# Performance work log

Hardware: AMD Instinct MI355X
Metric: run time of the kernel (lower is better)

The kernel has to match this reference:

```python
import jax, jax.numpy as jnp
import numpy as np

EPS = 1e-5
NH = 8          # num_heads
WT_LEVELS = 5


def ln(x, w, b):
    m = jnp.mean(x, -1, keepdims=True)
    v = jnp.mean((x - m) ** 2, -1, keepdims=True)
    return (x - m) / jnp.sqrt(v + EPS) * w + b


def gelu(x):
    return jax.nn.gelu(x, approximate=False)  # torch nn.GELU default (erf)


def dwconv(x, w, b, stride, padding):
    # x: [B,C,H,W], w: [kh,kw,1,C] depthwise
    C = x.shape[1]
    y = jax.lax.conv_general_dilated(x, w, (stride, stride), padding,
                                     dimension_numbers=('NCHW', 'HWIO', 'NCHW'),
                                     feature_group_count=C)
    return y if b is None else y + b[None, :, None, None]


def conv2d(x, w, b, padding='SAME'):
    y = jax.lax.conv_general_dilated(x, w, (1, 1), padding,
                                     dimension_numbers=('NCHW', 'HWIO', 'NCHW'))
    return y + b[None, :, None, None]


def haar_dwt(x):
    # orthonormal 2x2 Haar analysis via even/odd slicing (no conv needed)
    a = x[..., 0::2, 0::2]; b = x[..., 0::2, 1::2]
    c = x[..., 1::2, 0::2]; d = x[..., 1::2, 1::2]
    ll = (a + b + c + d) * 0.5
    lh = (-a - b + c + d) * 0.5
    hl = (-a + b - c + d) * 0.5
    hh = (a - b - c + d) * 0.5
    return ll, lh, hl, hh


def haar_idwt(ll, lh, hl, hh):
    a = (ll - lh - hl + hh) * 0.5
    b = (ll - lh + hl - hh) * 0.5
    c = (ll + lh - hl - hh) * 0.5
    d = (ll + lh + hl + hh) * 0.5
    B, C, H, W = ll.shape
    top = jnp.stack([a, b], -1).reshape(B, C, H, 2 * W)
    bot = jnp.stack([c, d], -1).reshape(B, C, H, 2 * W)
    return jnp.stack([top, bot], -2).reshape(B, C, 2 * H, 2 * W)


def wtconv(x, base_w, base_b, base_scale, wav_w, wav_scale):
    # WTConv2d (Haar, wt_levels=5, kernel 3, depthwise): multi-level wavelet
    # decomposition, depthwise 3x3 conv + scale at each level, reconstruction,
    # added to a scaled depthwise base conv.
    B, C = x.shape[0], x.shape[1]
    lls, hs, shapes = [], [], []
    cur = x
    for i in range(WT_LEVELS):
        shapes.append(cur.shape)
        Hc, Wc = cur.shape[2], cur.shape[3]
        if Hc % 2 or Wc % 2:
            cur = jnp.pad(cur, ((0, 0), (0, 0), (0, Hc % 2), (0, Wc % 2)))
        sub = jnp.stack(haar_dwt(cur), 2)                # [B,C,4,h,w]
        cur = sub[:, :, 0]
        h, w = sub.shape[3], sub.shape[4]
        t = sub.reshape(B, C * 4, h, w)
        t = dwconv(t, wav_w[i], None, 1, 'SAME') * wav_scale[i][None, :, None, None]
        t = t.reshape(B, C, 4, h, w)
        lls.append(t[:, :, 0])
        hs.append(t[:, :, 1:4])
    nxt = 0.0
    for i in range(WT_LEVELS - 1, -1, -1):
        ll = lls[i] + nxt
        h3 = hs[i]
        nxt = haar_idwt(ll, h3[:, :, 0], h3[:, :, 1], h3[:, :, 2])
        sh = shapes[i]
        nxt = nxt[:, :, :sh[2], :sh[3]]
    base = dwconv(x, base_w, base_b, 1, 'SAME') * base_scale[None, :, None, None]
    return base + nxt


def block_forward(x, H, W, ln1_w, ln1_b, ln2_w, ln2_b, q_w, kv1_w, kv2_w,
                  sr1_w, sr1_b, sr2_w, sr2_b, an1_w, an1_b, an2_w, an2_b,
                  wt_base_w, wt_base_b, wt_base_scale, wt_wav_w, wt_wav_scale,
                  cp2d_w, cp2d_b, cn_w, cn_b, proj_w, proj_b,
                  fc1_w, fc1_b, fc2_w, fc2_b):
    B, N, C0 = x.shape
    Cp = C0 // 4            # conv/wavelet part channels
    Ca = C0 - Cp            # attention part channels (3/4)
    hd = Ca // NH
    scale = hd ** -0.5

    xin = ln(x, ln1_w, ln1_b)
    xc, xa = xin[..., :Cp], xin[..., Cp:]

    # --- wavelet-conv branch ---
    xc = xc.reshape(B, H, W, Cp).transpose(0, 3, 1, 2)        # [B,Cp,H,W]
    xc = wtconv(xc, wt_base_w, wt_base_b, wt_base_scale, wt_wav_w, wt_wav_scale)
    xc = conv2d(xc, cp2d_w, cp2d_b, 'SAME')                   # k3 p1 (sr_ratio=8)
    xc = gelu(ln(xc.reshape(B, Cp, N).transpose(0, 2, 1), cn_w, cn_b))  # [B,N,Cp]

    # --- multi-scale spatial-reduction attention (sr_ratio=8) ---
    q = (xa @ q_w).reshape(B, N, NH, hd).transpose(0, 2, 1, 3)  # [B,NH,N,hd]
    x_ = xa.transpose(0, 2, 1).reshape(B, Ca, H, W)
    x1 = gelu(ln(dwconv(x_, sr1_w, sr1_b, 8, 'VALID').reshape(B, Ca, -1)
                 .transpose(0, 2, 1), an1_w, an1_b))           # [B,49,Ca]
    x2 = gelu(ln(dwconv(x_, sr2_w, sr2_b, 4, 'VALID').reshape(B, Ca, -1)
                 .transpose(0, 2, 1), an2_w, an2_b))           # [B,196,Ca]

    def branch(xs, kv_w, qh):
        L = xs.shape[1]
        kv = (xs @ kv_w).reshape(B, L, 2, NH // 2, hd).transpose(2, 0, 3, 1, 4)
        k, v = kv[0], kv[1]
        a = jax.nn.softmax(jnp.einsum('bhnd,bhld->bhnl', qh, k) * scale, axis=-1)
        return jnp.einsum('bhnl,bhld->bhnd', a, v).transpose(0, 2, 1, 3).reshape(B, N, Ca // 2)

    y1 = branch(x1, kv1_w, q[:, :NH // 2])
    y2 = branch(x2, kv2_w, q[:, NH // 2:])

    attn_out = jnp.concatenate([y1, y2, xc], -1) @ proj_w + proj_b

    x = x + attn_out
    m = ln(x, ln2_w, ln2_b)
    return x + (gelu(m @ fc1_w + fc1_b) @ fc2_w + fc2_b)


def setup_inputs() -> dict:
    key = jax.random.key(0)
    ks = jax.random.split(key, 16)
    B, H, W, C0 = 32, 56, 56, 128
    N = H * W
    Cp, Ca = C0 // 4, C0 // 4 * 3

    def nrm(k, shape, std=0.02):
        return jax.random.normal(k, shape, jnp.float32) * std

    return dict(
        x=jax.random.normal(ks[0], (B, N, C0), jnp.float32),
        H=H, W=W,
        ln1_w=jnp.ones((C0,)), ln1_b=jnp.zeros((C0,)),
        ln2_w=jnp.ones((C0,)), ln2_b=jnp.zeros((C0,)),
        q_w=nrm(ks[1], (Ca, Ca)),
        kv1_w=nrm(ks[2], (Ca, Ca)),
        kv2_w=nrm(ks[3], (Ca, Ca)),
        sr1_w=nrm(ks[4], (8, 8, 1, Ca), 0.05), sr1_b=jnp.zeros((Ca,)),
        sr2_w=nrm(ks[5], (4, 4, 1, Ca), 0.05), sr2_b=jnp.zeros((Ca,)),
        an1_w=jnp.ones((Ca,)), an1_b=jnp.zeros((Ca,)),
        an2_w=jnp.ones((Ca,)), an2_b=jnp.zeros((Ca,)),
        wt_base_w=nrm(ks[6], (3, 3, 1, Cp), 0.1), wt_base_b=jnp.zeros((Cp,)),
        wt_base_scale=jnp.ones((Cp,)),
        wt_wav_w=nrm(ks[7], (5, 3, 3, 1, 4 * Cp), 0.1),
        wt_wav_scale=jnp.full((5, 4 * Cp), 0.1, jnp.float32),
        cp2d_w=nrm(ks[8], (3, 3, Cp, Cp), 0.05), cp2d_b=jnp.zeros((Cp,)),
        cn_w=jnp.ones((Cp,)), cn_b=jnp.zeros((Cp,)),
        proj_w=nrm(ks[9], (C0, C0)), proj_b=jnp.zeros((C0,)),
        fc1_w=nrm(ks[10], (C0, 4 * C0)), fc1_b=jnp.zeros((4 * C0,)),
        fc2_w=nrm(ks[11], (4 * C0, C0)), fc2_b=jnp.zeros((C0,)),
    )


def reference(x, H, W, ln1_w, ln1_b, ln2_w, ln2_b, q_w, kv1_w, kv2_w,
              sr1_w, sr1_b, sr2_w, sr2_b, an1_w, an1_b, an2_w, an2_b,
              wt_base_w, wt_base_b, wt_base_scale, wt_wav_w, wt_wav_scale,
              cp2d_w, cp2d_b, cn_w, cn_b, proj_w, proj_b,
              fc1_w, fc1_b, fc2_w, fc2_b):
    return block_forward(x, H, W, ln1_w, ln1_b, ln2_w, ln2_b, q_w, kv1_w, kv2_w,
                         sr1_w, sr1_b, sr2_w, sr2_b, an1_w, an1_b, an2_w, an2_b,
                         wt_base_w, wt_base_b, wt_base_scale, wt_wav_w, wt_wav_scale,
                         cp2d_w, cp2d_b, cn_w, cn_b, proj_w, proj_b,
                         fc1_w, fc1_b, fc2_w, fc2_b)
```

## Files before the change

kernel.cpp:

```cpp
#include <hip/hip_runtime.h>
#include <hip/hip_bf16.h>
#include <math.h>

typedef __hip_bfloat16 bf16;
typedef __attribute__((ext_vector_type(8))) short bf16x8;
typedef __attribute__((ext_vector_type(4))) float f32x4;

#define Bc   32
#define Hc   56
#define Wcc  56
#define Nc   3136
#define Cpc  32
#define Cac  96
#define EPSc 1e-5f
#define SCALEc 0.28867513459481287f

__device__ __forceinline__ float gelu_f(float x) {
    return 0.5f * x * (1.0f + erff(x * 0.7071067811865475f));
}

__device__ __forceinline__ float fast_exp2(float x) {
#if defined(__has_builtin)
#if __has_builtin(__builtin_amdgcn_exp2f)
    return __builtin_amdgcn_exp2f(x);
#else
    return exp2f(x);
#endif
#else
    return exp2f(x);
#endif
}

__global__ __launch_bounds__(256) void ln1_kernel(const float* __restrict__ x,
        const float* __restrict__ g, const float* __restrict__ be,
        float* __restrict__ xa, bf16* __restrict__ xab, float* __restrict__ xc_img)
{
    int wv = threadIdx.x >> 6, lane = threadIdx.x & 63;
    int row = blockIdx.x * 4 + wv;
    if (row >= Bc * Nc) return;
    const float* xr = x + (size_t)row * 128;
    float x0 = xr[lane];
    float x1 = xr[lane + 64];
    float s = x0 + x1, q = x0 * x0 + x1 * x1;
    for (int o = 32; o; o >>= 1) { s += __shfl_xor(s, o); q += __shfl_xor(q, o); }
    float mean = s * (1.f / 128.f);
    float inv = rsqrtf(q * (1.f / 128.f) - mean * mean + EPSc);
    int b = row / Nc, n = row % Nc;
    {
        int c = lane;
        float y = (x0 - mean) * inv * g[c] + be[c];
        if (c < Cpc) xc_img[(size_t)(b * Cpc + c) * Nc + n] = y;
        else { xa[(size_t)row * Cac + (c - Cpc)] = y;
               xab[(size_t)row * Cac + (c - Cpc)] = __float2bfloat16(y); }
    }
    {
        int c = lane + 64;
        float y = (x1 - mean) * inv * g[c] + be[c];
        xa[(size_t)row * Cac + (c - Cpc)] = y;
        xab[(size_t)row * Cac + (c - Cpc)] = __float2bfloat16(y);
    }
}

__global__ void dwt_kernel(const float* __restrict__ src, int cs, int h, int w,
                           int h2, int w2, float* __restrict__ sub)
{
    int t = blockIdx.x * blockDim.x + threadIdx.x;
    int total = Bc * 32 * h2 * w2;
    if (t >= total) return;
    int xx = t % w2; int r = t / w2;
    int yy = r % h2; r /= h2;
    int c = r & 31; int b = r >> 5;
    const float* sp = src + (size_t)cs * (b * 32 + c) * h * w;
    int y0 = yy * 2, x0 = xx * 2;
    bool xe = (x0 + 1 < w), ye = (y0 + 1 < h);
    float a  = sp[y0 * w + x0];
    float bb = xe ? sp[y0 * w + x0 + 1] : 0.f;
    float cc = ye ? sp[(y0 + 1) * w + x0] : 0.f;
    float dd = (xe && ye) ? sp[(y0 + 1) * w + x0 + 1] : 0.f;
    size_t pl = (size_t)h2 * w2;
    size_t ob = (size_t)(b * 128 + c * 4) * pl + yy * w2 + xx;
    sub[ob]          = ( a + bb + cc + dd) * 0.5f;
    sub[ob + pl]     = (-a - bb + cc + dd) * 0.5f;
    sub[ob + 2 * pl] = (-a + bb - cc + dd) * 0.5f;
    sub[ob + 3 * pl] = ( a - bb - cc + dd) * 0.5f;
}

template<int H>
__device__ __forceinline__ void dw3_body(int r, const float* __restrict__ src,
        const float* __restrict__ wt, const float* __restrict__ scale,
        float* __restrict__ dst)
{
    int x = r % H; int rr = r / H;
    int y = rr % H; rr /= H;
    int c = rr & 127;
    const float* sp = src + (r - x - y * H);
    float acc = 0.f;
    #pragma unroll
    for (int u = 0; u < 3; u++) {
        int yy = y + u - 1;
        if (yy < 0 || yy >= H) continue;
        #pragma unroll
        for (int v = 0; v < 3; v++) {
            int xx = x + v - 1;
            if (xx < 0 || xx >= H) continue;
            acc += sp[yy * H + xx] * wt[(u * 3 + v) * 128 + c];
        }
    }
    dst[r] = acc * scale[c];
}

__global__ void dw3x3_all_kernel(const float* __restrict__ sub, const float* __restrict__ wavw,
        const float* __restrict__ wavs, float* __restrict__ tt)
{
    int t = blockIdx.x * blockDim.x + threadIdx.x;
    if (t < 3211264)      dw3_body<28>(t,           sub,           wavw,        wavs,       tt);
    else if (t < 4014080) dw3_body<14>(t - 3211264, sub + 3211264, wavw + 1152, wavs + 128, tt + 3211264);
    else if (t < 4214784) dw3_body<7> (t - 4014080, sub + 4014080, wavw + 2304, wavs + 256, tt + 4014080);
    else if (t < 4280320) dw3_body<4> (t - 4214784, sub + 4214784, wavw + 3456, wavs + 384, tt + 4214784);
    else if (t < 4296704) dw3_body<2> (t - 4280320, sub + 4280320, wavw + 4608, wavs + 512, tt + 4280320);
}

__global__ void idwt_kernel(const float* __restrict__ tl, const float* __restrict__ nxt,
        float* __restrict__ outp, int h2, int w2, int ho, int wo)
{
    int t = blockIdx.x * blockDim.x + threadIdx.x;
    int total = Bc * 32 * ho * wo;
    if (t >= total) return;
    int x = t % wo; int r = t / wo;
    int y = r % ho; r /= ho;
    int c = r & 31; int b = r >> 5;
    int y2 = y >> 1, x2 = x >> 1;
    size_t pl = (size_t)h2 * w2;
    size_t base = (size_t)(b * 128 + c * 4) * pl + y2 * w2 + x2;
    float ll = tl[base];
    if (nxt) ll += nxt[(size_t)(b * 32 + c) * pl + y2 * w2 + x2];
    float lh = tl[base + pl], hl = tl[base + 2 * pl], hh = tl[base + 3 * pl];
    float v;
    if ((y & 1) == 0) v = ((x & 1) == 0) ? (ll - lh - hl + hh) : (ll - lh + hl - hh);
    else              v = ((x & 1) == 0) ? (ll + lh - hl - hh) : (ll + lh + hl + hh);
    outp[t] = v * 0.5f;
}

__global__ void idwt_dwbase_kernel(const float* __restrict__ tl, const float* __restrict__ nxt,
        const float* __restrict__ src, const float* __restrict__ wt,
        const float* __restrict__ scale, const float* __restrict__ bias,
        bf16* __restrict__ dst_nhwc)
{
    int t = blockIdx.x * blockDim.x + threadIdx.x;
    if (t >= Bc * 32 * Nc) return;
    int x = t % Wcc; int r = t / Wcc;
    int y = r % Hc; r /= Hc;
    int c = r & 31; int b = r >> 5;
    int y2 = y >> 1, x2 = x >> 1;
    const size_t pl = 784;
    size_t base = (size_t)(b * 128 + c * 4) * pl + y2 * 28 + x2;
    float ll = tl[base] + nxt[(size_t)(b * 32 + c) * pl + y2 * 28 + x2];
    float lh = tl[base + pl], hl = tl[base + 2 * pl], hh = tl[base + 3 * pl];
    float v;
    if ((y & 1) == 0) v = ((x & 1) == 0) ? (ll - lh - hl + hh) : (ll - lh + hl - hh);
    else              v = ((x & 1) == 0) ? (ll + lh - hl - hh) : (ll + lh + hl + hh);
    float recon = v * 0.5f;
    const float* sp = src + (t - x - y * Wcc);
    float acc = 0.f;
    #pragma unroll
    for (int u = 0; u < 3; u++) {
        int yy = y + u - 1;
        if (yy < 0 || yy >= Hc) continue;
        #pragma unroll
        for (int vv2 = 0; vv2 < 3; vv2++) {
            int xx = x + vv2 - 1;
            if (xx < 0 || xx >= Wcc) continue;
            acc += sp[yy * Wcc + xx] * wt[(u * 3 + vv2) * 32 + c];
        }
    }
    acc = (acc + bias[c]) * scale[c] + recon;
    dst_nhwc[(((size_t)b * Hc + y) * Wcc + x) * 32 + c] = __float2bfloat16(acc);
}

__global__ void wprep_kernel(const float* __restrict__ qw, const float* __restrict__ kv1w,
        const float* __restrict__ kv2w, const float* __restrict__ pw,
        const float* __restrict__ f1w, const float* __restrict__ f2w,
        const float* __restrict__ cpw, bf16* __restrict__ qwt, bf16* __restrict__ kv1wt,
        bf16* __restrict__ kv2wt, bf16* __restrict__ pwt, bf16* __restrict__ w1t,
        bf16* __restrict__ w2t, bf16* __restrict__ cpwt)
{
    int t = blockIdx.x * blockDim.x + threadIdx.x;
    if (t < 9216) {
        int n = t % 96, k = t / 96;
        qwt[n * 96 + k] = __float2bfloat16(qw[t]);
    } else if (t < 18432) {
        int u = t - 9216; int n = u % 96, k = u / 96;
        kv1wt[n * 96 + k] = __float2bfloat16(kv1w[u]);
    } else if (t < 27648) {
        int u = t - 18432; int n = u % 96, k = u / 96;
        kv2wt[n * 96 + k] = __float2bfloat16(kv2w[u]);
    } else if (t < 44032) {
        int u = t - 27648; int n = u % 128, k = u / 128;
        pwt[n * 128 + k] = __float2bfloat16(pw[u]);
    } else if (t < 109568) {
        int u = t - 44032; int n = u % 512, k = u / 512;
        w1t[(size_t)n * 128 + k] = __float2bfloat16(f1w[u]);
    } else if (t < 175104) {
        int u = t - 109568; int n = u % 128, k = u / 128;
        w2t[(size_t)n * 512 + k] = __float2bfloat16(f2w[u]);
    } else if (t < 184320) {
        int u = t - 175104; int co = u / 288, k = u % 288;
        cpwt[u] = __float2bfloat16(cpw[k * 32 + co]);
    }
}

__global__ __launch_bounds__(256) void cp2d_cn_kernel(const bf16* __restrict__ src,
        const bf16* __restrict__ wtc, const float* __restrict__ bias,
        const float* __restrict__ cnw, const float* __restrict__ cnb,
        bf16* __restrict__ attn_cat)
{
    __shared__ unsigned short in_s[10 * 400];
    __shared__ unsigned short w_s[32 * 296];
    int tid = threadIdx.x;
    int b = blockIdx.y;
    int ty = blockIdx.x / 7, tx = blockIdx.x % 7;
    for (int idx = tid; idx < 1152; idx += 256) {
        int co = idx / 36, j8 = (idx % 36) * 8;
        *(int4*)&w_s[co * 296 + j8] = *(const int4*)(wtc + co * 288 + j8);
    }
    {
        int idx = tid;
        if (idx < 200) {
            int cell = idx >> 1, half = idx & 1;
            int dy = cell / 10, dx = cell % 10;
            int gy = ty * 8 - 1 + dy, gx = tx * 8 - 1 + dx;
            int4 v0 = make_int4(0, 0, 0, 0), v1 = v0;
            if (gy >= 0 && gy < 56 && gx >= 0 && gx < 56) {
                const int4* gp = (const int4*)(src + ((((size_t)b * 56 + gy) * 56 + gx) * 32 + half * 16));
                v0 = gp[0]; v1 = gp[1];
            }
            *(int4*)&in_s[dy * 400 + dx * 40 + half * 16] = v0;
            *(int4*)&in_s[dy * 400 + dx * 40 + half * 16 + 8] = v1;
        }
    }
    __syncthreads();
    int wave = tid >> 6, lane = tid & 63;
    int ml = lane & 15, qd = lane >> 4;
    int m = wave * 16 + ml;
    int ly = m >> 3, lx = m & 7;
    f32x4 acc0 = {0.f, 0.f, 0.f, 0.f}, acc1 = {0.f, 0.f, 0.f, 0.f};
    #pragma unroll
    for (int u = 0; u < 3; u++)
    #pragma unroll
    for (int v = 0; v < 3; v++) {
        bf16x8 af = *(const bf16x8*)&in_s[(ly + u) * 400 + (lx + v) * 40 + qd * 8];
        int k = (u * 3 + v) * 32 + qd * 8;
        bf16x8 b0 = *(const bf16x8*)&w_s[ml * 296 + k];
        bf16x8 b1 = *(const bf16x8*)&w_s[(16 + ml) * 296 + k];
        acc0 = __builtin_amdgcn_mfma_f32_16x16x32_bf16(af, b0, acc0, 0, 0, 0);
        acc1 = __builtin_amdgcn_mfma_f32_16x16x32_bf16(af, b1, acc1, 0, 0, 0);
    }
    float bia0 = bias[ml], bia1 = bias[16 + ml];
    float g0 = cnw[ml], g1 = cnw[16 + ml];
    float be0 = cnb[ml], be1 = cnb[16 + ml];
    #pragma unroll
    for (int r = 0; r < 4; r++) {
        float c0 = acc0[r] + bia0;
        float c1 = acc1[r] + bia1;
        float s = c0 + c1, q = c0 * c0 + c1 * c1;
        #pragma unroll
        for (int o = 8; o; o >>= 1) { s += __shfl_xor(s, o); q += __shfl_xor(q, o); }
        float mean = s * (1.f / 32.f);
        float inv = rsqrtf(q * (1.f / 32.f) - mean * mean + EPSc);
        int mr = wave * 16 + qd * 4 + r;
        int ry = ty * 8 + (mr >> 3), rx = tx * 8 + (mr & 7);
        bf16* op = attn_cat + ((size_t)b * Nc + ry * 56 + rx) * 128 + 96;
        op[ml]      = __float2bfloat16(gelu_f((c0 - mean) * inv * g0 + be0));
        op[16 + ml] = __float2bfloat16(gelu_f((c1 - mean) * inv * g1 + be1));
    }
}

template<int KS, int LD>
__device__ __forceinline__ void sr_body(int t, const float* __restrict__ xa,
        const float* __restrict__ wt, const float* __restrict__ bias,
        float* __restrict__ outp)
{
    int c = t % Cac; int r = t / Cac;
    int j = r % LD; r /= LD;
    int i = r % LD; int b = r / LD;
    float acc = bias[c];
    for (int u = 0; u < KS; u++)
        for (int v = 0; v < KS; v++)
            acc += xa[(size_t)(b * Nc + (i * KS + u) * Wcc + (j * KS + v)) * Cac + c]
                 * wt[(u * KS + v) * Cac + c];
    outp[t] = acc;
}

__global__ void sr_all_kernel(const float* __restrict__ xa,
        const float* __restrict__ sr1w, const float* __restrict__ sr1b, float* __restrict__ x1p,
        const float* __restrict__ sr2w, const float* __restrict__ sr2b, float* __restrict__ x2p)
{
    int t = blockIdx.x * blockDim.x + threadIdx.x;
    if (t < 150528) sr_body<8, 7>(t, xa, sr1w, sr1b, x1p);
    else {
        int u = t - 150528;
        if (u < 602112) sr_body<4, 14>(u, xa, sr2w, sr2b, x2p);
    }
}

__global__ __launch_bounds__(256) void ln96_all_kernel(
        const float* __restrict__ s1, const float* __restrict__ g1,
        const float* __restrict__ b1, bf16* __restrict__ d1,
        const float* __restrict__ s2, const float* __restrict__ g2,
        const float* __restrict__ b2, bf16* __restrict__ d2)
{
    int wv = threadIdx.x >> 6, lane = threadIdx.x & 63;
    int row = blockIdx.x * 4 + wv;
    const float* sp; const float* g; const float* be; bf16* dst; int r;
    if (row < 1568)      { sp = s1; g = g1; be = b1; dst = d1; r = row; }
    else if (row < 7840) { sp = s2; g = g2; be = b2; dst = d2; r = row - 1568; }
    else return;
    sp += (size_t)r * 96;
    float x0 = sp[lane];
    float x1 = (lane < 32) ? sp[64 + lane] : 0.f;
    float s = x0 + x1, q = x0 * x0 + x1 * x1;
    for (int o = 32; o; o >>= 1) { s += __shfl_xor(s, o); q += __shfl_xor(q, o); }
    float mean = s * (1.f / 96.f);
    float inv = rsqrtf(q * (1.f / 96.f) - mean * mean + EPSc);
    dst[(size_t)r * 96 + lane] =
        __float2bfloat16(gelu_f((x0 - mean) * inv * g[lane] + be[lane]));
    if (lane < 32)
        dst[(size_t)r * 96 + 64 + lane] =
            __float2bfloat16(gelu_f((x1 - mean) * inv * g[64 + lane] + be[64 + lane]));
}

template<int NF, int BK, bool GELU, bool RES, int OMODE>
__global__ __launch_bounds__(256) void gemm_kernel(const bf16* __restrict__ A,
        const bf16* __restrict__ Wt, const float* __restrict__ bias,
        const float* __restrict__ res, void* __restrict__ outp,
        int M, int K, int Nt)
{
    constexpr int TN = 16 * NF;
    __shared__ unsigned short As[64][BK + 8];
    __shared__ unsigned short Bs[TN][BK + 8];
    int tid = threadIdx.x;
    int wave = tid >> 6, lane = tid & 63;
    int m0 = blockIdx.y * 64, n0 = blockIdx.x * TN;
    f32x4 acc[NF];
    #pragma unroll
    for (int f = 0; f < NF; f++) acc[f] = (f32x4){0.f, 0.f, 0.f, 0.f};

    int ar = tid >> 2, ac = (tid & 3) << 3;
    int ml = wave * 16 + (lane & 15);
    int qd = lane >> 4;

    for (int k0 = 0; k0 < K; k0 += BK) {
        #pragma unroll
        for (int i = 0; i < BK / 32; i++) {
            int cc = ac + i * 32;
            int4 av = make_int4(0, 0, 0, 0);
            if (m0 + ar < M) av = *(const int4*)(A + (size_t)(m0 + ar) * K + k0 + cc);
            *(int4*)&As[ar][cc] = av;
        }
        for (int idx = tid; idx < TN * (BK / 8); idx += 256) {
            int br = idx / (BK / 8), bc = (idx % (BK / 8)) * 8;
            *(int4*)&Bs[br][bc] = *(const int4*)(Wt + (size_t)(n0 + br) * K + k0 + bc);
        }
        __syncthreads();
        #pragma unroll
        for (int kk = 0; kk < BK / 32; kk++) {
            bf16x8 af = *(const bf16x8*)&As[ml][kk * 32 + qd * 8];
            #pragma unroll
            for (int f = 0; f < NF; f++) {
                bf16x8 bfv = *(const bf16x8*)&Bs[f * 16 + (lane & 15)][kk * 32 + qd * 8];
                acc[f] = __builtin_amdgcn_mfma_f32_16x16x32_bf16(af, bfv, acc[f], 0, 0, 0);
            }
        }
        __syncthreads();
    }
    #pragma unroll
    for (int f = 0; f < NF; f++) {
        int n = n0 + f * 16 + (lane & 15);
        #pragma unroll
        for (int r = 0; r < 4; r++) {
            int m = m0 + wave * 16 + qd * 4 + r;
            if (m >= M) continue;
            float v = acc[f][r];
            if (bias) v += bias[n];
            if (GELU) v = gelu_f(v);
            if (RES)  v += res[(size_t)m * Nt + n];
            if (OMODE == 1)
                ((bf16*)outp)[(size_t)m * Nt + n] = __float2bfloat16(v);
            else if (OMODE == 2) {
                int b = m / Nc, nn = m - b * Nc;
                int h = n / 12, d = n - h * 12;
                ((float*)outp)[(((size_t)(b * 8 + h)) * Nc + nn) * 12 + d] = v;
            } else
                ((float*)outp)[(size_t)m * Nt + n] = v;
        }
    }
}

__global__ __launch_bounds__(256) void proj_ln_kernel(const bf16* __restrict__ A,
        const bf16* __restrict__ Wt, const float* __restrict__ bias,
        const float* __restrict__ res, const float* __restrict__ g,
        const float* __restrict__ be, float* __restrict__ xres, bf16* __restrict__ xnb)
{
    __shared__ unsigned short As[64][72];
    __shared__ unsigned short Bs[128][72];
    int tid = threadIdx.x;
    int wave = tid >> 6, lane = tid & 63;
    int m0 = blockIdx.x * 64;
    f32x4 acc[8];
    #pragma unroll
    for (int f = 0; f < 8; f++) acc[f] = (f32x4){0.f, 0.f, 0.f, 0.f};

    int ar = tid >> 2, ac = (tid & 3) << 3;
    int ml = lane & 15, qd = lane >> 4;
    int mlw = wave * 16 + ml;

    for (int k0 = 0; k0 < 128; k0 += 64) {
        #pragma unroll
        for (int i = 0; i < 2; i++) {
            int cc = ac + i * 32;
            *(int4*)&As[ar][cc] = *(const int4*)(A + (size_t)(m0 + ar) * 128 + k0 + cc);
        }
        for (int idx = tid; idx < 1024; idx += 256) {
            int br = idx >> 3, bc = (idx & 7) * 8;
            *(int4*)&Bs[br][bc] = *(const int4*)(Wt + (size_t)br * 128 + k0 + bc);
        }
        __syncthreads();
        #pragma unroll
        for (int kk = 0; kk < 2; kk++) {
            bf16x8 af = *(const bf16x8*)&As[mlw][kk * 32 + qd * 8];
            #pragma unroll
            for (int f = 0; f < 8; f++) {
                bf16x8 bfv = *(const bf16x8*)&Bs[f * 16 + ml][kk * 32 + qd * 8];
                acc[f] = __builtin_amdgcn_mfma_f32_16x16x32_bf16(af, bfv, acc[f], 0, 0, 0);
            }
        }
        __syncthreads();
    }
    float bia[8], gg[8], bb[8];
    #pragma unroll
    for (int f = 0; f < 8; f++) {
        int n = f * 16 + ml;
        bia[f] = bias[n]; gg[f] = g[n]; bb[f] = be[n];
    }
    #pragma unroll
    for (int r = 0; r < 4; r++) {
        int m = m0 + wave * 16 + qd * 4 + r;
        float vv[8];
        float s = 0.f, q = 0.f;
        #pragma unroll
        for (int f = 0; f < 8; f++) {
            int n = f * 16 + ml;
            float v = acc[f][r] + bia[f] + res[(size_t)m * 128 + n];
            vv[f] = v; s += v; q += v * v;
        }
        #pragma unroll
        for (int o = 8; o; o >>= 1) { s += __shfl_xor(s, o); q += __shfl_xor(q, o); }
        float mean = s * (1.f / 128.f);
        float inv = rsqrtf(q * (1.f / 128.f) - mean * mean + EPSc);
        #pragma unroll
        for (int f = 0; f < 8; f++) {
            int n = f * 16 + ml;
            xres[(size_t)m * 128 + n] = vv[f];
            xnb[(size_t)m * 128 + n] =
                __float2bfloat16((vv[f] - mean) * inv * gg[f] + bb[f]);
        }
    }
}

template<int L>
__device__ __forceinline__ void attn_body(const float* __restrict__ qh,
        const float* __restrict__ kv, int hl, int h, int b,
        float* kb, float* vb, bf16* __restrict__ attn_cat)
{
    for (int idx = threadIdx.x; idx < L * 3; idx += 256) {
        int l = idx / 3, f = idx % 3;
        const float4* kp = (const float4*)(kv + (size_t)(b * L + l) * 96 + hl * 12) + f;
        float4 kk = kp[0];
        float4 vv = kp[12];
        *(float4*)&kb[l * 12 + f * 4] = kk;
        *(float4*)&vb[l * 12 + f * 4] = vv;
    }
    int n = blockIdx.x * 256 + threadIdx.x;
    bool act = (n < Nc);
    int nn = act ? n : (Nc - 1);
    const float4* qp = (const float4*)(qh + (((size_t)(b * 8 + h)) * Nc + nn) * 12);
    float4 q0 = qp[0], q1 = qp[1], q2 = qp[2];
    const float PRE = SCALEc * 1.4426950408889634f;
    q0.x *= PRE; q0.y *= PRE; q0.z *= PRE; q0.w *= PRE;
    q1.x *= PRE; q1.y *= PRE; q1.z *= PRE; q1.w *= PRE;
    q2.x *= PRE; q2.y *= PRE; q2.z *= PRE; q2.w *= PRE;
    __syncthreads();

    float den = 0.f;
    float o[12];
    #pragma unroll
    for (int d = 0; d < 12; d++) o[d] = 0.f;

    #pragma unroll 4
    for (int l = 0; l < L; l++) {
        const float4 k0 = *(const float4*)&kb[l * 12];
        const float4 k1 = *(const float4*)&kb[l * 12 + 4];
        const float4 k2 = *(const float4*)&kb[l * 12 + 8];
        float s0 = q0.x * k0.x + q0.y * k0.y + q0.z * k0.z + q0.w * k0.w;
        float s1 = q1.x * k1.x + q1.y * k1.y + q1.z * k1.z + q1.w * k1.w;
        float s2 = q2.x * k2.x + q2.y * k2.y + q2.z * k2.z + q2.w * k2.w;
        float e = fast_exp2(s0 + s1 + s2);
        den += e;
        const float4 v0 = *(const float4*)&vb[l * 12];
        const float4 v1 = *(const float4*)&vb[l * 12 + 4];
        const float4 v2 = *(const float4*)&vb[l * 12 + 8];
        o[0] += e * v0.x; o[1]  += e * v0.y; o[2]  += e * v0.z; o[3]  += e * v0.w;
        o[4] += e * v1.x; o[5]  += e * v1.y; o[6]  += e * v1.z; o[7]  += e * v1.w;
        o[8] += e * v2.x; o[9]  += e * v2.y; o[10] += e * v2.z; o[11] += e * v2.w;
    }
    if (act) {
        float rden = 1.f / den;
        bf16* op = attn_cat + (size_t)(b * Nc + n) * 128 + h * 12;
        #pragma unroll
        for (int d = 0; d < 12; d++) op[d] = __float2bfloat16(o[d] * rden);
    }
}

__global__ __launch_bounds__(256) void attn_kernel(const float* __restrict__ qh,
        const float* __restrict__ kv1, const float* __restrict__ kv2,
        bf16* __restrict__ attn_cat)
{
    __shared__ float kb[196 * 12];
    __shared__ float vb[196 * 12];
    int h = blockIdx.y, b = blockIdx.z;
    if (h < 4) attn_body<49> (qh, kv1, h,     h, b, kb, vb, attn_cat);
    else       attn_body<196>(qh, kv2, h - 4, h, b, kb, vb, attn_cat);
}

extern "C" void kernel_launch(void* const* d_in, const int* in_sizes, int n_in,
                              void* d_out, int out_size, void* d_ws, size_t ws_size,
                              hipStream_t stream)
{
    const float* x    = (const float*)d_in[0];
    const float* ln1w = (const float*)d_in[3];
    const float* ln1b = (const float*)d_in[4];
    const float* ln2w = (const float*)d_in[5];
    const float* ln2b = (const float*)d_in[6];
    const float* qw   = (const float*)d_in[7];
    const float* kv1w = (const float*)d_in[8];
    const float* kv2w = (const float*)d_in[9];
    const float* sr1w = (const float*)d_in[10];
    const float* sr1b = (const float*)d_in[11];
    const float* sr2w = (const float*)d_in[12];
    const float* sr2b = (const float*)d_in[13];
    const float* an1w = (const float*)d_in[14];
    const float* an1b = (const float*)d_in[15];
    const float* an2w = (const float*)d_in[16];
    const float* an2b = (const float*)d_in[17];
    const float* wbw  = (const float*)d_in[18];
    const float* wbb  = (const float*)d_in[19];
    const float* wbs  = (const float*)d_in[20];
    const float* wavw = (const float*)d_in[21];
    const float* wavs = (const float*)d_in[22];
    const float* cpw  = (const float*)d_in[23];
    const float* cpb  = (const float*)d_in[24];
    const float* cnw  = (const float*)d_in[25];
    const float* cnb  = (const float*)d_in[26];
    const float* pw   = (const float*)d_in[27];
    const float* pb   = (const float*)d_in[28];
    const float* f1w  = (const float*)d_in[29];
    const float* f1b  = (const float*)d_in[30];
    const float* f2w  = (const float*)d_in[31];
    const float* f2b  = (const float*)d_in[32];
    float* dout = (float*)d_out;
    float* ws = (float*)d_ws;

    float* XA    = ws;
    float* QB    = ws + 9633792;
    float* XRES  = ws;
    bf16*  XNb   = (bf16*)(ws + 12845056);
    bf16*  XAb   = (bf16*)(ws + 19267584);
    bf16*  ACATb = (bf16*)(ws + 24084480);
    float* XCI   = ws + 30507008;
    float* SUB   = ws + 33718272;
    float* TT    = ws + 38014976;
    float* RA    = ws + 42311680;
    float* RB    = ws + 45522944;
    float* X1P   = ws + 48734208;
    float* X2P   = ws + 48884736;
    bf16*  X1Bb  = (bf16*)(ws + 49486848);
    bf16*  X2Bb  = (bf16*)(ws + 49562112);
    float* KV1   = ws + 49863168;
    float* KV2   = ws + 50013696;
    bf16*  WTB   = (bf16*)(ws + 50615808);
    bf16*  qwt   = WTB;
    bf16*  kv1wt = WTB + 9216;
    bf16*  kv2wt = WTB + 18432;
    bf16*  pwt   = WTB + 27648;
    bf16*  w1t   = WTB + 44032;
    bf16*  w2t   = WTB + 109568;
    bf16*  cpwt  = WTB + 175104;
    bf16*  Hb    = (bf16*)(ws + 24084480);
    bf16*  CIMGb = (bf16*)SUB;
    float* S0 = SUB;            float* T0 = TT;
    float* S1 = SUB + 3211264;  float* T1 = TT + 3211264;
    float* S2 = SUB + 4014080;  float* T2 = TT + 4014080;
    float* S3 = SUB + 4214784;  float* T3 = TT + 4214784;
    float* S4 = SUB + 4280320;  float* T4 = TT + 4280320;

    wprep_kernel<<<720, 256, 0, stream>>>(qw, kv1w, kv2w, pw, f1w, f2w, cpw,
                                          qwt, kv1wt, kv2wt, pwt, w1t, w2t, cpwt);

    ln1_kernel<<<25088, 256, 0, stream>>>(x, ln1w, ln1b, XA, XAb, XCI);

    dwt_kernel<<<3136, 256, 0, stream>>>(XCI, 1, 56, 56, 28, 28, S0);
    dwt_kernel<<<784,  256, 0, stream>>>(S0, 4, 28, 28, 14, 14, S1);
    dwt_kernel<<<196,  256, 0, stream>>>(S1, 4, 14, 14, 7, 7,   S2);
    dwt_kernel<<<64,   256, 0, stream>>>(S2, 4, 7, 7,   4, 4,   S3);
    dwt_kernel<<<16,   256, 0, stream>>>(S3, 4, 4, 4,   2, 2,   S4);

    dw3x3_all_kernel<<<16784, 256, 0, stream>>>(SUB, wavw, wavs, TT);

    idwt_kernel<<<64,   256, 0, stream>>>(T4, nullptr, RA, 2, 2, 4, 4);
    idwt_kernel<<<196,  256, 0, stream>>>(T3, RA, RB, 4, 4, 7, 7);
    idwt_kernel<<<784,  256, 0, stream>>>(T2, RB, RA, 7, 7, 14, 14);
    idwt_kernel<<<3136, 256, 0, stream>>>(T1, RA, RB, 14, 14, 28, 28);

    idwt_dwbase_kernel<<<12544, 256, 0, stream>>>(T0, RB, XCI, wbw, wbs, wbb, CIMGb);

    cp2d_cn_kernel<<<dim3(49, 32), 256, 0, stream>>>(CIMGb, cpwt, cpb, cnw, cnb, ACATb);

    sr_all_kernel<<<2940, 256, 0, stream>>>(XA, sr1w, sr1b, X1P, sr2w, sr2b, X2P);

    ln96_all_kernel<<<1960, 256, 0, stream>>>(X1P, an1w, an1b, X1Bb,
                                              X2P, an2w, an2b, X2Bb);

    gemm_kernel<6,32,false,false,2><<<dim3(1, 1568), 256, 0, stream>>>(XAb,  qwt,   nullptr, nullptr, QB,  100352, 96, 96);
    gemm_kernel<6,32,false,false,0><<<dim3(1, 25),   256, 0, stream>>>(X1Bb, kv1wt, nullptr, nullptr, KV1, 1568,   96, 96);
    gemm_kernel<6,32,false,false,0><<<dim3(1, 98),   256, 0, stream>>>(X2Bb, kv2wt, nullptr, nullptr, KV2, 6272,   96, 96);

    attn_kernel<<<dim3(13, 8, 32), 256, 0, stream>>>(QB, KV1, KV2, ACATb);

    proj_ln_kernel<<<1568, 256, 0, stream>>>(ACATb, pwt, pb, x, ln2w, ln2b, XRES, XNb);

    gemm_kernel<4,64,true,false,1><<<dim3(8, 1568), 256, 0, stream>>>(XNb, w1t, f1b, nullptr, Hb, 100352, 128, 512);

    gemm_kernel<4,64,false,true,0><<<dim3(2, 1568), 256, 0, stream>>>(Hb, w2t, f2b, XRES, dout, 100352, 512, 128);
}
```

Baseline: 607.3 us.

## Fuse MLP fc1+GELU and fc2 into one kernel keeping hidden in LDS

```diff
diff --git a/kernel.cpp b/kernel.cpp
--- a/kernel.cpp
+++ b/kernel.cpp
@@ -463,6 +463,94 @@
             xres[(size_t)m * 128 + n] = vv[f];
             xnb[(size_t)m * 128 + n] =
                 __float2bfloat16((vv[f] - mean) * inv * gg[f] + bb[f]);
+        }
+    }
+}
+
+__global__ __launch_bounds__(256) void fc12_kernel(const bf16* __restrict__ A,
+        const bf16* __restrict__ w1t, const float* __restrict__ f1b,
+        const bf16* __restrict__ w2t, const float* __restrict__ f2b,
+        const float* __restrict__ xres, float* __restrict__ dout)
+{
+    __shared__ unsigned short Hs[32][520];
+    __shared__ unsigned short Bbuf[9216];
+    int tid = threadIdx.x;
+    int wave = tid >> 6, lane = tid & 63;
+    int mw = wave & 1, nw = wave >> 1;
+    int ml = lane & 15, qd = lane >> 4;
+    int m0 = blockIdx.x * 32;
+
+    const bf16* arow = A + (size_t)(m0 + mw * 16 + ml) * 128;
+    bf16x8 af0 = *(const bf16x8*)(arow + qd * 8);
+    bf16x8 af1 = *(const bf16x8*)(arow + 32 + qd * 8);
+    bf16x8 af2 = *(const bf16x8*)(arow + 64 + qd * 8);
+    bf16x8 af3 = *(const bf16x8*)(arow + 96 + qd * 8);
+
+    for (int c = 0; c < 8; c++) {
+        for (int idx = tid; idx < 1024; idx += 256) {
+            int br = idx >> 4, bc = (idx & 15) * 8;
+            *(int4*)&Bbuf[br * 136 + bc] = *(const int4*)(w1t + (size_t)(c * 64 + br) * 128 + bc);
+        }
+        __syncthreads();
+        f32x4 acc0 = {0.f, 0.f, 0.f, 0.f}, acc1 = {0.f, 0.f, 0.f, 0.f};
+        {
+            bf16x8 b0, b1;
+            b0 = *(const bf16x8*)&Bbuf[(nw * 32 + ml) * 136 + qd * 8];
+            b1 = *(const bf16x8*)&Bbuf[(nw * 32 + 16 + ml) * 136 + qd * 8];
+            acc0 = __builtin_amdgcn_mfma_f32_16x16x32_bf16(af0, b0, acc0, 0, 0, 0);
+            acc1 = __builtin_amdgcn_mfma_f32_16x16x32_bf16(af0, b1, acc1, 0, 0, 0);
+            b0 = *(const bf16x8*)&Bbuf[(nw * 32 + ml) * 136 + 32 + qd * 8];
+            b1 = *(const bf16x8*)&Bbuf[(nw * 32 + 16 + ml) * 136 + 32 + qd * 8];
+            acc0 = __builtin_amdgcn_mfma_f32_16x16x32_bf16(af1, b0, acc0, 0, 0, 0);
+            acc1 = __builtin_amdgcn_mfma_f32_16x16x32_bf16(af1, b1, acc1, 0, 0, 0);
+            b0 = *(const bf16x8*)&Bbuf[(nw * 32 + ml) * 136 + 64 + qd * 8];
+            b1 = *(const bf16x8*)&Bbuf[(nw * 32 + 16 + ml) * 136 + 64 + qd * 8];
+            acc0 = __builtin_amdgcn_mfma_f32_16x16x32_bf16(af2, b0, acc0, 0, 0, 0);
+            acc1 = __builtin_amdgcn_mfma_f32_16x16x32_bf16(af2, b1, acc1, 0, 0, 0);
+            b0 = *(const bf16x8*)&Bbuf[(nw * 32 + ml) * 136 + 96 + qd * 8];
+            b1 = *(const bf16x8*)&Bbuf[(nw * 32 + 16 + ml) * 136 + 96 + qd * 8];
+            acc0 = __builtin_amdgcn_mfma_f32_16x16x32_bf16(af3, b0, acc0, 0, 0, 0);
+            acc1 = __builtin_amdgcn_mfma_f32_16x16x32_bf16(af3, b1, acc1, 0, 0, 0);
+        }
+        int n0l = c * 64 + nw * 32;
+        float bb0 = f1b[n0l + ml], bb1 = f1b[n0l + 16 + ml];
+        #pragma unroll
+        for (int r = 0; r < 4; r++) {
+            int hr = mw * 16 + qd * 4 + r;
+            *(bf16*)&Hs[hr][n0l + ml]      = __float2bfloat16(gelu_f(acc0[r] + bb0));
+            *(bf16*)&Hs[hr][n0l + 16 + ml] = __float2bfloat16(gelu_f(acc1[r] + bb1));
+        }
+        __syncthreads();
+    }
+
+    f32x4 acc[4];
+    #pragma unroll
+    for (int f = 0; f < 4; f++) acc[f] = (f32x4){0.f, 0.f, 0.f, 0.f};
+    for (int k0 = 0; k0 < 512; k0 += 64) {
+        for (int idx = tid; idx < 1024; idx += 256) {
+            int br = idx >> 3, bc = (idx & 7) * 8;
+            *(int4*)&Bbuf[br * 72 + bc] = *(const int4*)(w2t + (size_t)br * 512 + k0 + bc);
+        }
+        __syncthreads();
+        #pragma unroll
+        for (int kk = 0; kk < 2; kk++) {
+            bf16x8 ha = *(const bf16x8*)&Hs[mw * 16 + ml][k0 + kk * 32 + qd * 8];
+            #pragma unroll
+            for (int f = 0; f < 4; f++) {
+                bf16x8 bv = *(const bf16x8*)&Bbuf[(nw * 64 + f * 16 + ml) * 72 + kk * 32 + qd * 8];
+                acc[f] = __builtin_amdgcn_mfma_f32_16x16x32_bf16(ha, bv, acc[f], 0, 0, 0);
+            }
+        }
+        __syncthreads();
+    }
+    #pragma unroll
+    for (int f = 0; f < 4; f++) {
+        int n = nw * 64 + f * 16 + ml;
+        float bia = f2b[n];
+        #pragma unroll
+        for (int r = 0; r < 4; r++) {
+            int m = m0 + mw * 16 + qd * 4 + r;
+            dout[(size_t)m * 128 + n] = acc[f][r] + bia + xres[(size_t)m * 128 + n];
         }
     }
 }
@@ -595,7 +683,6 @@
     bf16*  w1t   = WTB + 44032;
     bf16*  w2t   = WTB + 109568;
     bf16*  cpwt  = WTB + 175104;
-    bf16*  Hb    = (bf16*)(ws + 24084480);
     bf16*  CIMGb = (bf16*)SUB;
     float* S0 = SUB;            float* T0 = TT;
     float* S1 = SUB + 3211264;  float* T1 = TT + 3211264;
@@ -638,7 +725,5 @@
 
     proj_ln_kernel<<<1568, 256, 0, stream>>>(ACATb, pwt, pb, x, ln2w, ln2b, XRES, XNb);
 
-    gemm_kernel<4,64,true,false,1><<<dim3(8, 1568), 256, 0, stream>>>(XNb, w1t, f1b, nullptr, Hb, 100352, 128, 512);
-
-    gemm_kernel<4,64,false,true,0><<<dim3(2, 1568), 256, 0, stream>>>(Hb, w2t, f2b, XRES, dout, 100352, 512, 128);
-}
+    fc12_kernel<<<3136, 256, 0, stream>>>(XNb, w1t, f1b, w2t, f2b, XRES, dout);
+}
```

New measurement: 607.5 us. Within noise of the previous version (+0.0%).

## Fuse small-level wavelet DWT/IDWT stages and widen fc2 GEMM tile

Applied to the files above, without the earlier changes.

```diff
diff --git a/kernel.cpp b/kernel.cpp
--- a/kernel.cpp
+++ b/kernel.cpp
@@ -85,6 +85,65 @@
     sub[ob + 3 * pl] = ( a - bb - cc + dd) * 0.5f;
 }
 
+__global__ __launch_bounds__(256) void dwt234_kernel(const float* __restrict__ S1,
+        float* __restrict__ S2, float* __restrict__ S3, float* __restrict__ S4)
+{
+    __shared__ float ll[196];
+    int bc = blockIdx.x; int b = bc >> 5, c = bc & 31;
+    int t = threadIdx.x;
+    const float* src = S1 + (size_t)(b * 128 + c * 4) * 196;
+    if (t < 196) ll[t] = src[t];
+    __syncthreads();
+    float l2 = 0.f;
+    if (t < 49) {
+        int yy = t / 7, xx = t % 7;
+        int y0 = yy * 2, x0 = xx * 2;
+        float a = ll[y0 * 14 + x0],       bb = ll[y0 * 14 + x0 + 1];
+        float cc = ll[(y0 + 1) * 14 + x0], dd = ll[(y0 + 1) * 14 + x0 + 1];
+        size_t ob = (size_t)(b * 128 + c * 4) * 49 + t;
+        float vll = (a + bb + cc + dd) * 0.5f;
+        S2[ob]       = vll;
+        S2[ob + 49]  = (-a - bb + cc + dd) * 0.5f;
+        S2[ob + 98]  = (-a + bb - cc + dd) * 0.5f;
+        S2[ob + 147] = ( a - bb - cc + dd) * 0.5f;
+        l2 = vll;
+    }
+    __syncthreads();
+    if (t < 49) ll[t] = l2;
+    __syncthreads();
+    float l3 = 0.f;
+    if (t < 16) {
+        int yy = t >> 2, xx = t & 3;
+        int y0 = yy * 2, x0 = xx * 2;
+        bool xe = (x0 + 1 < 7), ye = (y0 + 1 < 7);
+        float a  = ll[y0 * 7 + x0];
+        float bb = xe ? ll[y0 * 7 + x0 + 1] : 0.f;
+        float cc = ye ? ll[(y0 + 1) * 7 + x0] : 0.f;
+        float dd = (xe && ye) ? ll[(y0 + 1) * 7 + x0 + 1] : 0.f;
+        size_t ob = (size_t)(b * 128 + c * 4) * 16 + t;
+        float vll = (a + bb + cc + dd) * 0.5f;
+        S3[ob]      = vll;
+        S3[ob + 16] = (-a - bb + cc + dd) * 0.5f;
+        S3[ob + 32] = (-a + bb - cc + dd) * 0.5f;
+        S3[ob + 48] = ( a - bb - cc + dd) * 0.5f;
+        l3 = vll;
+    }
+    __syncthreads();
+    if (t < 16) ll[t] = l3;
+    __syncthreads();
+    if (t < 4) {
+        int yy = t >> 1, xx = t & 1;
+        int y0 = yy * 2, x0 = xx * 2;
+        float a = ll[y0 * 4 + x0],       bb = ll[y0 * 4 + x0 + 1];
+        float cc = ll[(y0 + 1) * 4 + x0], dd = ll[(y0 + 1) * 4 + x0 + 1];
+        size_t ob = (size_t)(b * 128 + c * 4) * 4 + t;
+        S4[ob]      = ( a + bb + cc + dd) * 0.5f;
+        S4[ob + 4]  = (-a - bb + cc + dd) * 0.5f;
+        S4[ob + 8]  = (-a + bb - cc + dd) * 0.5f;
+        S4[ob + 12] = ( a - bb - cc + dd) * 0.5f;
+    }
+}
+
 template<int H>
 __device__ __forceinline__ void dw3_body(int r, const float* __restrict__ src,
         const float* __restrict__ wt, const float* __restrict__ scale,
@@ -118,6 +177,55 @@
     else if (t < 4214784) dw3_body<7> (t - 4014080, sub + 4014080, wavw + 2304, wavs + 256, tt + 4014080);
     else if (t < 4280320) dw3_body<4> (t - 4214784, sub + 4214784, wavw + 3456, wavs + 384, tt + 4214784);
     else if (t < 4296704) dw3_body<2> (t - 4280320, sub + 4280320, wavw + 4608, wavs + 512, tt + 4280320);
+}
+
+__global__ __launch_bounds__(256) void idwt432_kernel(const float* __restrict__ T4,
+        const float* __restrict__ T3, const float* __restrict__ T2,
+        float* __restrict__ out14)
+{
+    __shared__ float rec[196];
+    int bc = blockIdx.x; int b = bc >> 5, c = bc & 31;
+    int t = threadIdx.x;
+    float v4 = 0.f;
+    if (t < 16) {
+        int y = t >> 2, x = t & 3;
+        int y2 = y >> 1, x2 = x >> 1;
+        size_t base = (size_t)(b * 128 + c * 4) * 4 + y2 * 2 + x2;
+        float ll = T4[base];
+        float lh = T4[base + 4], hl = T4[base + 8], hh = T4[base + 12];
+        float v;
+        if ((y & 1) == 0) v = ((x & 1) == 0) ? (ll - lh - hl + hh) : (ll - lh + hl - hh);
+        else              v = ((x & 1) == 0) ? (ll + lh - hl - hh) : (ll + lh + hl + hh);
+        v4 = v * 0.5f;
+    }
+    if (t < 16) rec[t] = v4;
+    __syncthreads();
+    float v3 = 0.f;
+    if (t < 49) {
+        int y = t / 7, x = t % 7;
+        int y2 = y >> 1, x2 = x >> 1;
+        size_t base = (size_t)(b * 128 + c * 4) * 16 + y2 * 4 + x2;
+        float ll = T3[base] + rec[y2 * 4 + x2];
+        float lh = T3[base + 16], hl = T3[base + 32], hh = T3[base + 48];
+        float v;
+        if ((y & 1) == 0) v = ((x & 1) == 0) ? (ll - lh - hl + hh) : (ll - lh + hl - hh);
+        else              v = ((x & 1) == 0) ? (ll + lh - hl - hh) : (ll + lh + hl + hh);
+        v3 = v * 0.5f;
+    }
+    __syncthreads();
+    if (t < 49) rec[t] = v3;
+    __syncthreads();
+    if (t < 196) {
+        int y = t / 14, x = t % 14;
+        int y2 = y >> 1, x2 = x >> 1;
+        size_t base = (size_t)(b * 128 + c * 4) * 49 + y2 * 7 + x2;
+        float ll = T2[base] + rec[y2 * 7 + x2];
+        float lh = T2[base + 49], hl = T2[base + 98], hh = T2[base + 147];
+        float v;
+        if ((y & 1) == 0) v = ((x & 1) == 0) ? (ll - lh - hl + hh) : (ll - lh + hl - hh);
+        else              v = ((x & 1) == 0) ? (ll + lh - hl - hh) : (ll + lh + hl + hh);
+        out14[(size_t)(b * 32 + c) * 196 + t] = v * 0.5f;
+    }
 }
 
 __global__ void idwt_kernel(const float* __restrict__ tl, const float* __restrict__ nxt,
@@ -610,15 +718,11 @@
 
     dwt_kernel<<<3136, 256, 0, stream>>>(XCI, 1, 56, 56, 28, 28, S0);
     dwt_kernel<<<784,  256, 0, stream>>>(S0, 4, 28, 28, 14, 14, S1);
-    dwt_kernel<<<196,  256, 0, stream>>>(S1, 4, 14, 14, 7, 7,   S2);
-    dwt_kernel<<<64,   256, 0, stream>>>(S2, 4, 7, 7,   4, 4,   S3);
-    dwt_kernel<<<16,   256, 0, stream>>>(S3, 4, 4, 4,   2, 2,   S4);
+    dwt234_kernel<<<1024, 256, 0, stream>>>(S1, S2, S3, S4);
 
     dw3x3_all_kernel<<<16784, 256, 0, stream>>>(SUB, wavw, wavs, TT);
 
-    idwt_kernel<<<64,   256, 0, stream>>>(T4, nullptr, RA, 2, 2, 4, 4);
-    idwt_kernel<<<196,  256, 0, stream>>>(T3, RA, RB, 4, 4, 7, 7);
-    idwt_kernel<<<784,  256, 0, stream>>>(T2, RB, RA, 7, 7, 14, 14);
+    idwt432_kernel<<<1024, 256, 0, stream>>>(T4, T3, T2, RA);
     idwt_kernel<<<3136, 256, 0, stream>>>(T1, RA, RB, 14, 14, 28, 28);
 
     idwt_dwbase_kernel<<<12544, 256, 0, stream>>>(T0, RB, XCI, wbw, wbs, wbb, CIMGb);
@@ -640,5 +744,5 @@
 
     gemm_kernel<4,64,true,false,1><<<dim3(8, 1568), 256, 0, stream>>>(XNb, w1t, f1b, nullptr, Hb, 100352, 128, 512);
 
-    gemm_kernel<4,64,false,true,0><<<dim3(2, 1568), 256, 0, stream>>>(Hb, w2t, f2b, XRES, dout, 100352, 512, 128);
-}
+    gemm_kernel<8,64,false,true,0><<<dim3(1, 1568), 256, 0, stream>>>(Hb, w2t, f2b, XRES, dout, 100352, 512, 128);
+}
```

Result: no change. 619.1 us (+1.9%).
